# Kernel optimization log

Hardware: AMD Instinct MI355X
Metric: run time of the kernel (lower is better)

Reference implementation:

```python
import jax, jax.numpy as jnp
import numpy as np

N_NODES = 100000
N_EDGES = 1600000
N_FEAT = 128
HIDDEN = 64
N_CLASSES = 40


def setup_inputs() -> dict:
    key = jax.random.key(0)
    ks = jax.random.split(key, 4)
    x = jax.random.normal(ks[0], (N_NODES, N_FEAT), dtype=jnp.float32)
    edge_index = jax.random.randint(ks[1], (2, N_EDGES), 0, N_NODES, dtype=jnp.int64)
    # Glorot-style init like PyG GCNConv
    W1 = jax.random.normal(ks[2], (N_FEAT, HIDDEN), dtype=jnp.float32) * (1.0 / np.sqrt(N_FEAT))
    b1 = jnp.zeros((HIDDEN,), dtype=jnp.float32)
    W2 = jax.random.normal(ks[3], (HIDDEN, N_CLASSES), dtype=jnp.float32) * (1.0 / np.sqrt(HIDDEN))
    b2 = jnp.zeros((N_CLASSES,), dtype=jnp.float32)
    return {"x": x, "edge_index": edge_index, "W1": W1, "b1": b1, "W2": W2, "b2": b2}


def _gcn_conv(x, src, dst, norm, W, b, n_nodes):
    # PyG GCNConv: transform first, then normalized scatter-add aggregation
    h = x @ W                                   # [N, out]
    msg = h[src] * norm[:, None]                # [E+N, out] gather
    out = jax.ops.segment_sum(msg, dst, num_segments=n_nodes)  # scatter-add
    return out + b


def _norm_and_loops(edge_index, n_nodes):
    # add self-loops, symmetric normalization deg^{-1/2} A_hat deg^{-1/2}
    loop = jnp.arange(n_nodes, dtype=edge_index.dtype)
    src = jnp.concatenate([edge_index[0], loop])
    dst = jnp.concatenate([edge_index[1], loop])
    deg = jax.ops.segment_sum(jnp.ones_like(dst, dtype=jnp.float32), dst, num_segments=n_nodes)
    dinv = jnp.where(deg > 0, jax.lax.rsqrt(jnp.maximum(deg, 1.0)), 0.0)
    norm = dinv[src] * dinv[dst]
    return src, dst, norm


def reference(x, edge_index, W1, b1, W2, b2):
    n_nodes = x.shape[0]
    src, dst, norm = _norm_and_loops(edge_index, n_nodes)
    h = _gcn_conv(x, src, dst, norm, W1, b1, n_nodes)
    h = jax.nn.relu(h)
    h = _gcn_conv(h, src, dst, norm, W2, b2, n_nodes)
    return jax.nn.log_softmax(h, axis=1)
```

## Files before the change

### kernel.cpp

```cpp
#include <hip/hip_runtime.h>
#include <hip/hip_bf16.h>
#include <string.h>

#define N_FEAT 128
#define HIDDEN 64
#define N_CLS  40
#define FILL_BLOCKS 2048
#define CHUNK_EDGES 8192
#define B_BITS 6
#define SRC_BITS 17

typedef __bf16 bf16x8 __attribute__((ext_vector_type(8)));
typedef float  f32x4  __attribute__((ext_vector_type(4)));

union Frag { unsigned u[4]; bf16x8 v; };

static __device__ inline int get_xcc() {
    return (int)(__builtin_amdgcn_s_getreg((3 << 11) | 20) & 7u);
}


static __device__ inline unsigned pack_bf16(float a, float b) {
    unsigned ba = __float_as_uint(a);
    unsigned bb = __float_as_uint(b);
    unsigned ra = (ba + 0x7fffu + ((ba >> 16) & 1u)) >> 16;
    unsigned rb = (bb + 0x7fffu + ((bb >> 16) & 1u)) >> 16;
    return (ra & 0xffffu) | (rb << 16);
}

static __device__ inline float2 unpack_bf16(unsigned v) {
    return make_float2(__uint_as_float(v << 16), __uint_as_float(v & 0xffff0000u));
}


__global__ void detect_layout_kernel(const int* __restrict__ ei, int* __restrict__ flag) {
    int lane = threadIdx.x;
    int v = ei[2 * lane + 1];
    unsigned long long b = __ballot(v != 0);
    if (lane == 0) flag[0] = (b == 0ull) ? 1 : 0;
}


__global__ __launch_bounds__(256) void bucket_hist_kernel(const int* __restrict__ ei,
                                                          const int* __restrict__ flag,
                                                          unsigned* __restrict__ bcnt8,
                                                          int E, int nbuk) {
    __shared__ unsigned h[2048];
    for (int i = threadIdx.x; i < nbuk; i += 256) h[i] = 0u;
    __syncthreads();
    bool is64 = (flag[0] != 0);
    if (is64) {
        int idx = blockIdx.x * 256 + threadIdx.x;
        int stride2 = gridDim.x * 256 * 2;
        int Eeven = E & ~1;
        for (int e = idx * 2; e < Eeven; e += stride2) {
            uint4 dv = *(const uint4*)(ei + (size_t)2 * E + (size_t)2 * e);
            atomicAdd(&h[((int)dv.x) >> B_BITS], 1u);
            atomicAdd(&h[((int)dv.z) >> B_BITS], 1u);
        }
        for (int e = Eeven + idx; e < E; e += gridDim.x * 256) {
            int d = ei[(size_t)2 * E + (size_t)2 * e];
            atomicAdd(&h[d >> B_BITS], 1u);
        }
    } else {
        const int* dstp = ei + E;
        for (int e = blockIdx.x * 256 + threadIdx.x; e < E; e += gridDim.x * 256) {
            int d = dstp[e];
            atomicAdd(&h[d >> B_BITS], 1u);
        }
    }
    __syncthreads();
    unsigned copy = (blockIdx.x & 7u) << 11;
    for (int i = threadIdx.x; i < nbuk; i += 256)
        if (h[i]) atomicAdd(&bcnt8[copy + i], h[i]);
}


__global__ __launch_bounds__(512) void bucket_scan_kernel(const unsigned* __restrict__ bcnt8,
                                                          unsigned* __restrict__ bbase,
                                                          unsigned* __restrict__ bcur, int nbuk) {
    __shared__ unsigned tmp[512];
    __shared__ unsigned carry;
    if (threadIdx.x == 0) carry = 0u;
    __syncthreads();
    for (int base = 0; base < nbuk; base += 512) {
        int i = base + threadIdx.x;
        unsigned v = 0u;
        if (i < nbuk) {
#pragma unroll
            for (int c = 0; c < 8; ++c) v += bcnt8[(c << 11) + i];
        }
        tmp[threadIdx.x] = v;
        __syncthreads();
#pragma unroll
        for (int off = 1; off < 512; off <<= 1) {
            unsigned t = (threadIdx.x >= (unsigned)off) ? tmp[threadIdx.x - off] : 0u;
            __syncthreads();
            tmp[threadIdx.x] += t;
            __syncthreads();
        }
        unsigned excl = tmp[threadIdx.x] - v + carry;
        if (i < nbuk) {
            bbase[i] = excl;
            bcur[(size_t)i * 16] = excl;
        }
        __syncthreads();
        if (threadIdx.x == 511) carry += tmp[511];
        __syncthreads();
    }
}


__global__ __launch_bounds__(256) void fill_buckets_kernel(const int* __restrict__ ei,
                                                           const int* __restrict__ flag,
                                                           unsigned* __restrict__ bcur,
                                                           unsigned* __restrict__ ctr,
                                                           unsigned* __restrict__ tmpbuf,
                                                           int E, int nbuk) {
    int r = get_xcc();
    int bpx = (nbuk + 7) >> 3;
    int blo = r * bpx;
    int bhi = min(nbuk, blo + bpx);
    int nlb = bhi - blo;
    bool is64 = (flag[0] != 0);
    const size_t dstoff = (size_t)2 * E;

    __shared__ unsigned hist[256], lbase[256], lcur[256];
    __shared__ unsigned chunk_s;

    for (;;) {
        if (threadIdx.x == 0)
            chunk_s = __hip_atomic_fetch_add(&ctr[r * 64], 1u, __ATOMIC_RELAXED,
                                             __HIP_MEMORY_SCOPE_WORKGROUP);
        if (threadIdx.x < 256) { hist[threadIdx.x] = 0u; lcur[threadIdx.x] = 0u; }
        __syncthreads();
        long long base = (long long)chunk_s * CHUNK_EDGES;
        if (base >= E) break;
        int end = (int)min((long long)E, base + CHUNK_EDGES);

        if (is64) {
            for (int e = (int)base + 2 * threadIdx.x; e + 1 < end; e += 512) {
                uint4 dv = *(const uint4*)(ei + dstoff + (size_t)2 * e);
                int b0 = ((int)dv.x) >> B_BITS;
                int b1 = ((int)dv.z) >> B_BITS;
                if (b0 >= blo && b0 < bhi) atomicAdd(&hist[b0 - blo], 1u);
                if (b1 >= blo && b1 < bhi) atomicAdd(&hist[b1 - blo], 1u);
            }
            if ((end - (int)base) & 1) {
                if (threadIdx.x == 0) {
                    int d = ei[dstoff + (size_t)2 * (end - 1)];
                    int b = d >> B_BITS;
                    if (b >= blo && b < bhi) atomicAdd(&hist[b - blo], 1u);
                }
            }
        } else {
            for (int e = (int)base + threadIdx.x; e < end; e += 256) {
                int b = ei[(size_t)E + e] >> B_BITS;
                if (b >= blo && b < bhi) atomicAdd(&hist[b - blo], 1u);
            }
        }
        __syncthreads();

        for (int lb = threadIdx.x; lb < nlb; lb += 256) {
            unsigned h = hist[lb];
            if (h) lbase[lb] = __hip_atomic_fetch_add(&bcur[(size_t)(blo + lb) * 16], h,
                                                      __ATOMIC_RELAXED, __HIP_MEMORY_SCOPE_WORKGROUP);
        }
        __syncthreads();

        if (is64) {
            for (int e = (int)base + 2 * threadIdx.x; e + 1 < end; e += 512) {
                uint4 dv = *(const uint4*)(ei + dstoff + (size_t)2 * e);
                {
                    int d = (int)dv.x;
                    int b = d >> B_BITS;
                    if (b >= blo && b < bhi) {
                        unsigned s = (unsigned)ei[(size_t)2 * e];
                        int lb = b - blo;
                        unsigned off = atomicAdd(&lcur[lb], 1u);
                        tmpbuf[lbase[lb] + off] =
                            ((unsigned)(d & ((1 << B_BITS) - 1)) << SRC_BITS) | s;
                    }
                }
                {
                    int d = (int)dv.z;
                    int b = d >> B_BITS;
                    if (b >= blo && b < bhi) {
                        unsigned s = (unsigned)ei[(size_t)2 * (e + 1)];
                        int lb = b - blo;
                        unsigned off = atomicAdd(&lcur[lb], 1u);
                        tmpbuf[lbase[lb] + off] =
                            ((unsigned)(d & ((1 << B_BITS) - 1)) << SRC_BITS) | s;
                    }
                }
            }
            if ((end - (int)base) & 1) {
                if (threadIdx.x == 0) {
                    int e = end - 1;
                    int d = ei[dstoff + (size_t)2 * e];
                    int b = d >> B_BITS;
                    if (b >= blo && b < bhi) {
                        int lb = b - blo;
                        unsigned off = atomicAdd(&lcur[lb], 1u);
                        tmpbuf[lbase[lb] + off] =
                            ((unsigned)(d & ((1 << B_BITS) - 1)) << SRC_BITS)
                            | (unsigned)ei[(size_t)2 * e];
                    }
                }
            }
        } else {
            for (int e = (int)base + threadIdx.x; e < end; e += 256) {
                int d = ei[(size_t)E + e];
                int b = d >> B_BITS;
                if (b >= blo && b < bhi) {
                    int lb = b - blo;
                    unsigned off = atomicAdd(&lcur[lb], 1u);
                    tmpbuf[lbase[lb] + off] =
                        ((unsigned)(d & ((1 << B_BITS) - 1)) << SRC_BITS) | (unsigned)ei[e];
                }
            }
        }
        __syncthreads();
    }
}


__global__ __launch_bounds__(256) void bucket_to_csr_kernel(const unsigned* __restrict__ tmpbuf,
                                                            const unsigned* __restrict__ bbase,
                                                            unsigned* __restrict__ deg,
                                                            unsigned* __restrict__ rowptr,
                                                            float* __restrict__ dinv,
                                                            int* __restrict__ csr_src,
                                                            int nbuk, int N, int E) {
    int b = blockIdx.x;
    int tid = threadIdx.x;
    unsigned beg = bbase[b];
    unsigned end = (b + 1 < nbuk) ? bbase[b + 1] : (unsigned)E;
    int d0 = b << B_BITS;
    const int ND = 1 << B_BITS;
    __shared__ unsigned hist[ND], scn[ND], cur[ND];
    if (tid < ND) { hist[tid] = 0u; cur[tid] = 0u; }
    __syncthreads();
    for (unsigned i = beg + tid; i < end; i += 256)
        atomicAdd(&hist[tmpbuf[i] >> SRC_BITS], 1u);
    __syncthreads();
    if (tid == 0) {
        unsigned run = 0;
        for (int k = 0; k < ND; ++k) { scn[k] = run; run += hist[k]; }
    }
    __syncthreads();
    if (tid < ND) {
        int d = d0 + tid;
        if (d < N) {
            unsigned dg = hist[tid];
            deg[d] = dg;
            dinv[d] = rsqrtf((float)(dg + 1u));
            rowptr[d] = beg + scn[tid];
        }
    }
    __syncthreads();
    for (unsigned i = beg + tid; i < end; i += 256) {
        unsigned v = tmpbuf[i];
        unsigned dl = v >> SRC_BITS;
        unsigned s = v & ((1u << SRC_BITS) - 1u);
        unsigned p = atomicAdd(&cur[dl], 1u);
        csr_src[beg + scn[dl] + p] = (int)s;
    }
}


__global__ __launch_bounds__(256) void gemm1_mfma_kernel(const float* __restrict__ x,
                                                         const float* __restrict__ W1,
                                                         const float* __restrict__ dinv,
                                                         unsigned* __restrict__ h1b, int N) {
    int lane = threadIdx.x & 63;
    int quad = lane >> 4;
    int col  = lane & 15;

    Frag B[4][4];
#pragma unroll
    for (int c = 0; c < 4; ++c)
#pragma unroll
        for (int ks = 0; ks < 4; ++ks) {
            int n = c * 16 + col;
#pragma unroll
            for (int jj = 0; jj < 4; ++jj) {
                int k = ks * 32 + quad * 8 + 2 * jj;
                B[c][ks].u[jj] = pack_bf16(W1[k * HIDDEN + n], W1[(k + 1) * HIDDEN + n]);
            }
        }

    int wave_id = blockIdx.x * 4 + (threadIdx.x >> 6);
    int nwaves  = gridDim.x * 4;
    int ntiles  = (N + 15) >> 4;

    for (int rt = wave_id; rt < ntiles; rt += nwaves) {
        int rowA = rt * 16 + col;
        Frag A[4];
#pragma unroll
        for (int ks = 0; ks < 4; ++ks) {
            float4 a0 = make_float4(0.f, 0.f, 0.f, 0.f), a1 = a0;
            if (rowA < N) {
                const float4* ap = (const float4*)(x + (size_t)rowA * N_FEAT + ks * 32 + quad * 8);
                a0 = ap[0];
                a1 = ap[1];
            }
            A[ks].u[0] = pack_bf16(a0.x, a0.y);
            A[ks].u[1] = pack_bf16(a0.z, a0.w);
            A[ks].u[2] = pack_bf16(a1.x, a1.y);
            A[ks].u[3] = pack_bf16(a1.z, a1.w);
        }
        f32x4 acc[4] = {{0.f, 0.f, 0.f, 0.f}, {0.f, 0.f, 0.f, 0.f},
                        {0.f, 0.f, 0.f, 0.f}, {0.f, 0.f, 0.f, 0.f}};
#pragma unroll
        for (int ks = 0; ks < 4; ++ks)
#pragma unroll
            for (int c = 0; c < 4; ++c)
                acc[c] = __builtin_amdgcn_mfma_f32_16x16x32_bf16(A[ks].v, B[c][ks].v, acc[c], 0, 0, 0);

        int rowD = rt * 16 + quad * 4;
#pragma unroll
        for (int c = 0; c < 4; ++c)
#pragma unroll
            for (int r = 0; r < 4; ++r) {
                float v = acc[c][r];
                float nxt = __shfl_down(v, 1);
                int row = rowD + r;
                if (((lane & 1) == 0) && row < N) {
                    float dr = dinv[row];
                    h1b[(size_t)row * 32 + ((c * 16 + col) >> 1)] = pack_bf16(v * dr, nxt * dr);
                }
            }
    }
}


__global__ __launch_bounds__(256) void gemm2_mfma_kernel(const unsigned* __restrict__ actb,
                                                         const float* __restrict__ W2,
                                                         const float* __restrict__ dinv,
                                                         unsigned* __restrict__ h2a,
                                                         unsigned* __restrict__ h2c, int N) {
    int lane = threadIdx.x & 63;
    int quad = lane >> 4;
    int col  = lane & 15;

    Frag B[3][2];
#pragma unroll
    for (int c = 0; c < 3; ++c)
#pragma unroll
        for (int ks = 0; ks < 2; ++ks) {
            int n = c * 16 + col;
#pragma unroll
            for (int jj = 0; jj < 4; ++jj) {
                int k = ks * 32 + quad * 8 + 2 * jj;
                float w0 = (n < N_CLS) ? W2[k * N_CLS + n] : 0.f;
                float w1 = (n < N_CLS) ? W2[(k + 1) * N_CLS + n] : 0.f;
                B[c][ks].u[jj] = pack_bf16(w0, w1);
            }
        }

    int wave_id = blockIdx.x * 4 + (threadIdx.x >> 6);
    int nwaves  = gridDim.x * 4;
    int ntiles  = (N + 15) >> 4;

    for (int rt = wave_id; rt < ntiles; rt += nwaves) {
        int rowA = rt * 16 + col;
        Frag A[2];
#pragma unroll
        for (int ks = 0; ks < 2; ++ks) {
            uint4 u = make_uint4(0u, 0u, 0u, 0u);
            if (rowA < N)
                u = *(const uint4*)(actb + (size_t)rowA * 32 + ks * 16 + quad * 4);
            A[ks].u[0] = u.x; A[ks].u[1] = u.y; A[ks].u[2] = u.z; A[ks].u[3] = u.w;
        }
        f32x4 acc[3] = {{0.f, 0.f, 0.f, 0.f}, {0.f, 0.f, 0.f, 0.f}, {0.f, 0.f, 0.f, 0.f}};
#pragma unroll
        for (int ks = 0; ks < 2; ++ks)
#pragma unroll
            for (int c = 0; c < 3; ++c)
                acc[c] = __builtin_amdgcn_mfma_f32_16x16x32_bf16(A[ks].v, B[c][ks].v, acc[c], 0, 0, 0);

        int rowD = rt * 16 + quad * 4;
#pragma unroll
        for (int c = 0; c < 3; ++c)
#pragma unroll
            for (int r = 0; r < 4; ++r) {
                float v = acc[c][r];
                float nxt = __shfl_down(v, 1);
                int row = rowD + r;
                int pair = (c * 16 + col) >> 1;
                if (((lane & 1) == 0) && row < N) {
                    float dr = dinv[row];
                    if (pair < 16)
                        h2a[(size_t)row * 16 + pair] = pack_bf16(v * dr, nxt * dr);
                    else if (pair < 20)
                        h2c[(size_t)row * 4 + (pair - 16)] = pack_bf16(v * dr, nxt * dr);
                }
            }
    }
}


__global__ __launch_bounds__(256) void agg1_kernel(const unsigned* __restrict__ h1b,
                                                   const int* __restrict__ csr_src,
                                                   const unsigned* __restrict__ rowptr,
                                                   const unsigned* __restrict__ deg,
                                                   const float* __restrict__ dinv,
                                                   const float* __restrict__ b1,
                                                   unsigned* __restrict__ actb, int N) {
    int wave = threadIdx.x >> 6, lane = threadIdx.x & 63;
    int sub = lane >> 5, j = lane & 31;
    int d = blockIdx.x * 4 + wave;
    if (d >= N) return;
    float dv = dinv[d];
    float acc0 = 0.f, acc1 = 0.f;
    if (sub == 0) {
        float2 v = unpack_bf16(h1b[(size_t)d * 32 + j]);
        acc0 = v.x; acc1 = v.y;
    }
    unsigned beg = rowptr[d];
    int len = (int)deg[d];
    int i = 0;
    for (; i + 16 <= len; i += 16) {
        int s0 = csr_src[beg + i + sub];
        int s1 = csr_src[beg + i + 2 + sub];
        int s2 = csr_src[beg + i + 4 + sub];
        int s3 = csr_src[beg + i + 6 + sub];
        int s4 = csr_src[beg + i + 8 + sub];
        int s5 = csr_src[beg + i + 10 + sub];
        int s6 = csr_src[beg + i + 12 + sub];
        int s7 = csr_src[beg + i + 14 + sub];
        unsigned v0 = h1b[(size_t)s0 * 32 + j];
        unsigned v1 = h1b[(size_t)s1 * 32 + j];
        unsigned v2 = h1b[(size_t)s2 * 32 + j];
        unsigned v3 = h1b[(size_t)s3 * 32 + j];
        unsigned v4 = h1b[(size_t)s4 * 32 + j];
        unsigned v5 = h1b[(size_t)s5 * 32 + j];
        unsigned v6 = h1b[(size_t)s6 * 32 + j];
        unsigned v7 = h1b[(size_t)s7 * 32 + j];
        float2 a0 = unpack_bf16(v0), a1 = unpack_bf16(v1);
        float2 a2 = unpack_bf16(v2), a3 = unpack_bf16(v3);
        float2 a4 = unpack_bf16(v4), a5 = unpack_bf16(v5);
        float2 a6 = unpack_bf16(v6), a7 = unpack_bf16(v7);
        acc0 += a0.x + a1.x + a2.x + a3.x + a4.x + a5.x + a6.x + a7.x;
        acc1 += a0.y + a1.y + a2.y + a3.y + a4.y + a5.y + a6.y + a7.y;
    }
    for (; i + 8 <= len; i += 8) {
        int s0 = csr_src[beg + i + sub];
        int s1 = csr_src[beg + i + 2 + sub];
        int s2 = csr_src[beg + i + 4 + sub];
        int s3 = csr_src[beg + i + 6 + sub];
        unsigned v0 = h1b[(size_t)s0 * 32 + j];
        unsigned v1 = h1b[(size_t)s1 * 32 + j];
        unsigned v2 = h1b[(size_t)s2 * 32 + j];
        unsigned v3 = h1b[(size_t)s3 * 32 + j];
        float2 a0 = unpack_bf16(v0), a1 = unpack_bf16(v1);
        float2 a2 = unpack_bf16(v2), a3 = unpack_bf16(v3);
        acc0 += a0.x + a1.x + a2.x + a3.x;
        acc1 += a0.y + a1.y + a2.y + a3.y;
    }
    for (; i + 4 <= len; i += 4) {
        int sA = csr_src[beg + i + sub];
        int sB = csr_src[beg + i + 2 + sub];
        float2 a = unpack_bf16(h1b[(size_t)sA * 32 + j]);
        float2 b = unpack_bf16(h1b[(size_t)sB * 32 + j]);
        acc0 += a.x + b.x;
        acc1 += a.y + b.y;
    }
    for (; i < len; i += 2) {
        int e = i + sub;
        if (e < len) {
            int s = csr_src[beg + e];
            float2 a = unpack_bf16(h1b[(size_t)s * 32 + j]);
            acc0 += a.x;
            acc1 += a.y;
        }
    }
    acc0 += __shfl_xor(acc0, 32);
    acc1 += __shfl_xor(acc1, 32);
    if (sub == 0) {
        float2 bb = ((const float2*)b1)[j];
        float r0 = fmaxf(acc0 * dv + bb.x, 0.f);
        float r1 = fmaxf(acc1 * dv + bb.y, 0.f);
        actb[(size_t)d * 32 + j] = pack_bf16(r0, r1);
    }
}


__global__ __launch_bounds__(256) void agg2_lsm_kernel(const unsigned* __restrict__ h2a,
                                                       const unsigned* __restrict__ h2c,
                                                       const int* __restrict__ csr_src,
                                                       const unsigned* __restrict__ rowptr,
                                                       const unsigned* __restrict__ deg,
                                                       const float* __restrict__ dinv,
                                                       const float* __restrict__ b2,
                                                       float* __restrict__ out, int N) {
    int wave = threadIdx.x >> 6, lane = threadIdx.x & 63;
    int sub = lane >> 5, j = lane & 31;
    bool act = (j < 20);
    const unsigned* tab;
    unsigned str;
    if (j < 16) { tab = h2a + j; str = 16u; }
    else        { tab = h2c + (j - 16); str = 4u; }
    int d = blockIdx.x * 4 + wave;
    if (d >= N) return;
    float dv = dinv[d];
    float acc0 = 0.f, acc1 = 0.f;
    if (sub == 0 && act) {
        float2 v = unpack_bf16(tab[(size_t)d * str]);
        acc0 = v.x; acc1 = v.y;
    }
    unsigned beg = rowptr[d];
    int len = (int)deg[d];
    int i = 0;
    for (; i + 16 <= len; i += 16) {
        int s0 = csr_src[beg + i + sub];
        int s1 = csr_src[beg + i + 2 + sub];
        int s2 = csr_src[beg + i + 4 + sub];
        int s3 = csr_src[beg + i + 6 + sub];
        int s4 = csr_src[beg + i + 8 + sub];
        int s5 = csr_src[beg + i + 10 + sub];
        int s6 = csr_src[beg + i + 12 + sub];
        int s7 = csr_src[beg + i + 14 + sub];
        if (act) {
            float2 a0 = unpack_bf16(tab[(size_t)s0 * str]);
            float2 a1 = unpack_bf16(tab[(size_t)s1 * str]);
            float2 a2 = unpack_bf16(tab[(size_t)s2 * str]);
            float2 a3 = unpack_bf16(tab[(size_t)s3 * str]);
            float2 a4 = unpack_bf16(tab[(size_t)s4 * str]);
            float2 a5 = unpack_bf16(tab[(size_t)s5 * str]);
            float2 a6 = unpack_bf16(tab[(size_t)s6 * str]);
            float2 a7 = unpack_bf16(tab[(size_t)s7 * str]);
            acc0 += a0.x + a1.x + a2.x + a3.x + a4.x + a5.x + a6.x + a7.x;
            acc1 += a0.y + a1.y + a2.y + a3.y + a4.y + a5.y + a6.y + a7.y;
        }
    }
    for (; i + 8 <= len; i += 8) {
        int s0 = csr_src[beg + i + sub];
        int s1 = csr_src[beg + i + 2 + sub];
        int s2 = csr_src[beg + i + 4 + sub];
        int s3 = csr_src[beg + i + 6 + sub];
        if (act) {
            float2 a0 = unpack_bf16(tab[(size_t)s0 * str]);
            float2 a1 = unpack_bf16(tab[(size_t)s1 * str]);
            float2 a2 = unpack_bf16(tab[(size_t)s2 * str]);
            float2 a3 = unpack_bf16(tab[(size_t)s3 * str]);
            acc0 += a0.x + a1.x + a2.x + a3.x;
            acc1 += a0.y + a1.y + a2.y + a3.y;
        }
    }
    for (; i + 4 <= len; i += 4) {
        int sA = csr_src[beg + i + sub];
        int sB = csr_src[beg + i + 2 + sub];
        if (act) {
            float2 a = unpack_bf16(tab[(size_t)sA * str]);
            float2 b = unpack_bf16(tab[(size_t)sB * str]);
            acc0 += a.x + b.x;
            acc1 += a.y + b.y;
        }
    }
    for (; i < len; i += 2) {
        int e = i + sub;
        if (e < len && act) {
            int s = csr_src[beg + e];
            float2 a = unpack_bf16(tab[(size_t)s * str]);
            acc0 += a.x;
            acc1 += a.y;
        }
    }
    acc0 += __shfl_xor(acc0, 32);
    acc1 += __shfl_xor(acc1, 32);
    float v0 = -1e30f, v1 = -1e30f;
    if (act) {
        float2 bb = ((const float2*)b2)[j];
        v0 = acc0 * dv + bb.x;
        v1 = acc1 * dv + bb.y;
    }
    float m = fmaxf(v0, v1);
#pragma unroll
    for (int off = 32; off > 0; off >>= 1)
        m = fmaxf(m, __shfl_xor(m, off));
    float ex = (act && sub == 0) ? (expf(v0 - m) + expf(v1 - m)) : 0.f;
#pragma unroll
    for (int off = 32; off > 0; off >>= 1)
        ex += __shfl_xor(ex, off);
    float ls = logf(ex);
    if (act && sub == 0) {
        float2* orow = (float2*)(out + (size_t)d * N_CLS);
        orow[j] = make_float2(v0 - m - ls, v1 - m - ls);
    }
}


static inline size_t align_up(size_t x) { return (x + 255) & ~(size_t)255; }

extern "C" void kernel_launch(void* const* d_in, const int* in_sizes, int n_in,
                              void* d_out, int out_size, void* d_ws, size_t ws_size,
                              hipStream_t stream) {
    const float* x  = (const float*)d_in[0];
    const int*   ei = (const int*)d_in[1];
    const float* W1 = (const float*)d_in[2];
    const float* b1 = (const float*)d_in[3];
    const float* W2 = (const float*)d_in[4];
    const float* b2 = (const float*)d_in[5];

    int N = in_sizes[0] / N_FEAT;
    int E = in_sizes[1] / 2;
    int nbuk = (N + (1 << B_BITS) - 1) >> B_BITS;

    char* ws = (char*)d_ws;
    int*      flag    = (int*)ws;       ws += 256;
    unsigned* ctrs    = (unsigned*)ws;  ws += 4096;
    unsigned* bcnt8   = (unsigned*)ws;  ws += 8 * 2048 * 4;
    unsigned* bbase   = (unsigned*)ws;  ws += align_up((size_t)nbuk * 4);
    unsigned* bcur    = (unsigned*)ws;  ws += align_up((size_t)nbuk * 64);
    unsigned* deg     = (unsigned*)ws;  ws += align_up((size_t)N * 4);
    float*    dinv    = (float*)ws;     ws += align_up((size_t)N * 4);
    unsigned* rowptr  = (unsigned*)ws;  ws += align_up((size_t)N * 4);
    unsigned* tmpbuf  = (unsigned*)ws;  ws += align_up((size_t)E * 4);
    int*      csr_src = (int*)ws;       ws += align_up((size_t)E * 4);
    unsigned* h1b     = (unsigned*)ws;  ws += align_up((size_t)N * 32 * 4);
    unsigned* actb    = (unsigned*)ws;  ws += align_up((size_t)N * 32 * 4);
    unsigned* h2a     = (unsigned*)ws;  ws += align_up((size_t)N * 16 * 4);
    unsigned* h2c     = (unsigned*)ws;  ws += align_up((size_t)N * 4 * 4);

    hipMemsetAsync(ctrs, 0, 4096 + 8 * 2048 * 4, stream);

    detect_layout_kernel<<<1, 64, 0, stream>>>(ei, flag);
    bucket_hist_kernel<<<256, 256, 0, stream>>>(ei, flag, bcnt8, E, nbuk);
    bucket_scan_kernel<<<1, 512, 0, stream>>>(bcnt8, bbase, bcur, nbuk);
    fill_buckets_kernel<<<FILL_BLOCKS, 256, 0, stream>>>(ei, flag, bcur, ctrs, tmpbuf, E, nbuk);
    bucket_to_csr_kernel<<<nbuk, 256, 0, stream>>>(tmpbuf, bbase, deg, rowptr, dinv, csr_src, nbuk, N, E);

    gemm1_mfma_kernel<<<512, 256, 0, stream>>>(x, W1, dinv, h1b, N);
    agg1_kernel<<<(N + 3) / 4, 256, 0, stream>>>(h1b, csr_src, rowptr, deg, dinv, b1, actb, N);

    gemm2_mfma_kernel<<<512, 256, 0, stream>>>(actb, W2, dinv, h2a, h2c, N);
    agg2_lsm_kernel<<<(N + 3) / 4, 256, 0, stream>>>(h2a, h2c, csr_src, rowptr, deg, dinv, b2, (float*)d_out, N);
}
```

Before: 321.9 us.

## Split layer-2 aggregation into two source-range passes for cache locality

Layer-2 aggregation now runs twice. The first pass gathers only sources in the lower half of the node range and writes fp32 partial sums. The second pass gathers the upper half, adds the partials, then applies bias and log-softmax. The aim is to keep each pass's gathered table slice resident in cache. In exchange, the CSR index list is read twice, a partial buffer must be written and read back, and per-edge branches are added.

```diff
diff --git a/kernel.cpp b/kernel.cpp
--- a/kernel.cpp
+++ b/kernel.cpp
@@ -487,14 +487,16 @@
 }
 
 
-__global__ __launch_bounds__(256) void agg2_lsm_kernel(const unsigned* __restrict__ h2a,
-                                                       const unsigned* __restrict__ h2c,
-                                                       const int* __restrict__ csr_src,
-                                                       const unsigned* __restrict__ rowptr,
-                                                       const unsigned* __restrict__ deg,
-                                                       const float* __restrict__ dinv,
-                                                       const float* __restrict__ b2,
-                                                       float* __restrict__ out, int N) {
+__global__ __launch_bounds__(256) void agg2_pass_kernel(int pass,
+                                                        const unsigned* __restrict__ h2a,
+                                                        const unsigned* __restrict__ h2c,
+                                                        const int* __restrict__ csr_src,
+                                                        const unsigned* __restrict__ rowptr,
+                                                        const unsigned* __restrict__ deg,
+                                                        const float* __restrict__ dinv,
+                                                        const float* __restrict__ b2,
+                                                        float2* __restrict__ partial,
+                                                        float* __restrict__ out, int N) {
     int wave = threadIdx.x >> 6, lane = threadIdx.x & 63;
     int sub = lane >> 5, j = lane & 31;
     bool act = (j < 20);
@@ -504,11 +506,18 @@
     else        { tab = h2c + (j - 16); str = 4u; }
     int d = blockIdx.x * 4 + wave;
     if (d >= N) return;
+    int half = (N + 1) >> 1;
+    bool p0 = (pass == 0);
     float dv = dinv[d];
     float acc0 = 0.f, acc1 = 0.f;
     if (sub == 0 && act) {
-        float2 v = unpack_bf16(tab[(size_t)d * str]);
-        acc0 = v.x; acc1 = v.y;
+        if (p0) {
+            float2 v = unpack_bf16(tab[(size_t)d * str]);
+            acc0 = v.x; acc1 = v.y;
+        } else {
+            float2 p = partial[(size_t)d * 20 + j];
+            acc0 = p.x; acc1 = p.y;
+        }
     }
     unsigned beg = rowptr[d];
     int len = (int)deg[d];
@@ -523,53 +532,33 @@
         int s6 = csr_src[beg + i + 12 + sub];
         int s7 = csr_src[beg + i + 14 + sub];
         if (act) {
-            float2 a0 = unpack_bf16(tab[(size_t)s0 * str]);
-            float2 a1 = unpack_bf16(tab[(size_t)s1 * str]);
-            float2 a2 = unpack_bf16(tab[(size_t)s2 * str]);
-            float2 a3 = unpack_bf16(tab[(size_t)s3 * str]);
-            float2 a4 = unpack_bf16(tab[(size_t)s4 * str]);
-            float2 a5 = unpack_bf16(tab[(size_t)s5 * str]);
-            float2 a6 = unpack_bf16(tab[(size_t)s6 * str]);
-            float2 a7 = unpack_bf16(tab[(size_t)s7 * str]);
-            acc0 += a0.x + a1.x + a2.x + a3.x + a4.x + a5.x + a6.x + a7.x;
-            acc1 += a0.y + a1.y + a2.y + a3.y + a4.y + a5.y + a6.y + a7.y;
-        }
-    }
-    for (; i + 8 <= len; i += 8) {
-        int s0 = csr_src[beg + i + sub];
-        int s1 = csr_src[beg + i + 2 + sub];
-        int s2 = csr_src[beg + i + 4 + sub];
-        int s3 = csr_src[beg + i + 6 + sub];
-        if (act) {
-            float2 a0 = unpack_bf16(tab[(size_t)s0 * str]);
-            float2 a1 = unpack_bf16(tab[(size_t)s1 * str]);
-            float2 a2 = unpack_bf16(tab[(size_t)s2 * str]);
-            float2 a3 = unpack_bf16(tab[(size_t)s3 * str]);
-            acc0 += a0.x + a1.x + a2.x + a3.x;
-            acc1 += a0.y + a1.y + a2.y + a3.y;
-        }
-    }
-    for (; i + 4 <= len; i += 4) {
-        int sA = csr_src[beg + i + sub];
-        int sB = csr_src[beg + i + 2 + sub];
-        if (act) {
-            float2 a = unpack_bf16(tab[(size_t)sA * str]);
-            float2 b = unpack_bf16(tab[(size_t)sB * str]);
-            acc0 += a.x + b.x;
-            acc1 += a.y + b.y;
+            if ((s0 < half) == p0) { float2 a = unpack_bf16(tab[(size_t)s0 * str]); acc0 += a.x; acc1 += a.y; }
+            if ((s1 < half) == p0) { float2 a = unpack_bf16(tab[(size_t)s1 * str]); acc0 += a.x; acc1 += a.y; }
+            if ((s2 < half) == p0) { float2 a = unpack_bf16(tab[(size_t)s2 * str]); acc0 += a.x; acc1 += a.y; }
+            if ((s3 < half) == p0) { float2 a = unpack_bf16(tab[(size_t)s3 * str]); acc0 += a.x; acc1 += a.y; }
+            if ((s4 < half) == p0) { float2 a = unpack_bf16(tab[(size_t)s4 * str]); acc0 += a.x; acc1 += a.y; }
+            if ((s5 < half) == p0) { float2 a = unpack_bf16(tab[(size_t)s5 * str]); acc0 += a.x; acc1 += a.y; }
+            if ((s6 < half) == p0) { float2 a = unpack_bf16(tab[(size_t)s6 * str]); acc0 += a.x; acc1 += a.y; }
+            if ((s7 < half) == p0) { float2 a = unpack_bf16(tab[(size_t)s7 * str]); acc0 += a.x; acc1 += a.y; }
         }
     }
     for (; i < len; i += 2) {
         int e = i + sub;
         if (e < len && act) {
             int s = csr_src[beg + e];
-            float2 a = unpack_bf16(tab[(size_t)s * str]);
-            acc0 += a.x;
-            acc1 += a.y;
+            if ((s < half) == p0) {
+                float2 a = unpack_bf16(tab[(size_t)s * str]);
+                acc0 += a.x; acc1 += a.y;
+            }
         }
     }
     acc0 += __shfl_xor(acc0, 32);
     acc1 += __shfl_xor(acc1, 32);
+    if (p0) {
+        if (sub == 0 && act)
+            partial[(size_t)d * 20 + j] = make_float2(acc0, acc1);
+        return;
+    }
     float v0 = -1e30f, v1 = -1e30f;
     if (act) {
         float2 bb = ((const float2*)b2)[j];
@@ -623,6 +612,7 @@
     unsigned* actb    = (unsigned*)ws;  ws += align_up((size_t)N * 32 * 4);
     unsigned* h2a     = (unsigned*)ws;  ws += align_up((size_t)N * 16 * 4);
     unsigned* h2c     = (unsigned*)ws;  ws += align_up((size_t)N * 4 * 4);
+    float2*   partial = (float2*)ws;    ws += align_up((size_t)N * 20 * 8);
 
     hipMemsetAsync(ctrs, 0, 4096 + 8 * 2048 * 4, stream);
 
@@ -636,5 +626,6 @@
     agg1_kernel<<<(N + 3) / 4, 256, 0, stream>>>(h1b, csr_src, rowptr, deg, dinv, b1, actb, N);
 
     gemm2_mfma_kernel<<<512, 256, 0, stream>>>(actb, W2, dinv, h2a, h2c, N);
-    agg2_lsm_kernel<<<(N + 3) / 4, 256, 0, stream>>>(h2a, h2c, csr_src, rowptr, deg, dinv, b2, (float*)d_out, N);
-}
+    agg2_pass_kernel<<<(N + 3) / 4, 256, 0, stream>>>(0, h2a, h2c, csr_src, rowptr, deg, dinv, b2, partial, (float*)d_out, N);
+    agg2_pass_kernel<<<(N + 3) / 4, 256, 0, stream>>>(1, h2a, h2c, csr_src, rowptr, deg, dinv, b2, partial, (float*)d_out, N);
+}
```

Result: slower. 401.3 us (+24.7%).
